# Kernel tuning notes

Measured on AMD Instinct MI355X. Metric: run time of the kernel, lower is better.

## Reference

```python
import jax, jax.numpy as jnp
import numpy as np

D_MODEL = 512
NHEAD = 4
HEAD_DIM = D_MODEL // NHEAD


def setup_inputs() -> dict:
    key = jax.random.key(0)
    ks = jax.random.split(key, 12)
    B, S = 2, 4096
    s = 1.0 / np.sqrt(D_MODEL)
    inp = {
        "query": jax.random.normal(ks[0], (B, S, D_MODEL), jnp.float32),
        "key": jax.random.normal(ks[1], (B, S, D_MODEL), jnp.float32),
        "value": jax.random.normal(ks[2], (B, S, D_MODEL), jnp.float32),
        "Wq": jax.random.uniform(ks[3], (D_MODEL, D_MODEL), jnp.float32, -s, s),
        "bq": jax.random.uniform(ks[4], (D_MODEL,), jnp.float32, -s, s),
        "Wk": jax.random.uniform(ks[5], (D_MODEL, D_MODEL), jnp.float32, -s, s),
        "bk": jax.random.uniform(ks[6], (D_MODEL,), jnp.float32, -s, s),
        "Wv": jax.random.uniform(ks[7], (D_MODEL, D_MODEL), jnp.float32, -s, s),
        "bv": jax.random.uniform(ks[8], (D_MODEL,), jnp.float32, -s, s),
        "Wo": jax.random.uniform(ks[9], (D_MODEL, D_MODEL), jnp.float32, -s, s),
        "bo": jax.random.uniform(ks[10], (D_MODEL,), jnp.float32, -s, s),
    }
    return inp


def reference(query, key, value, Wq, bq, Wk, bk, Wv, bv, Wo, bo):
    B, Sq, _ = query.shape
    Sk = key.shape[1]
    # projections (torch Linear: x @ W.T + b); split heads -> [B, H, S, hd]
    def proj(x, W, b, S):
        return (x @ W.T + b).reshape(B, S, NHEAD, HEAD_DIM).transpose(0, 2, 1, 3)
    Q = proj(query, Wq, bq, Sq)
    K = proj(key, Wk, bk, Sk)
    V = proj(value, Wv, bv, Sk)
    scale = 1.0 / np.sqrt(HEAD_DIM).astype(np.float32)
    scores = jnp.einsum("bhqd,bhkd->bhqk", Q, K) * scale  # [B,H,Sq,Sk]
    weights = jax.nn.softmax(scores, axis=-1)
    out = jnp.einsum("bhqk,bhkd->bhqd", weights, V)  # [B,H,Sq,hd]
    out = out.transpose(0, 2, 1, 3).reshape(B, Sq, D_MODEL)
    return out @ Wo.T + bo
```

## Files before the change

kernel.cpp:

```cpp
#include <hip/hip_runtime.h>


#define D_MODEL 512
#define NHEAD 4
#define HD 128
#define S_ 4096

typedef __attribute__((ext_vector_type(8))) short bf16x8;
typedef __attribute__((ext_vector_type(4))) short bf16x4;
typedef __attribute__((ext_vector_type(4))) float f32x4;
typedef __attribute__((ext_vector_type(2))) unsigned uint2v;
typedef __attribute__((ext_vector_type(4))) unsigned uint4v;

__device__ __forceinline__ short f2bf(float f) {
    unsigned u = __builtin_bit_cast(unsigned, f);
    u += 0x7fffu + ((u >> 16) & 1u);
    return (short)(u >> 16);
}
__device__ __forceinline__ unsigned pk2bf(float a, float b) {
    unsigned ua = __builtin_bit_cast(unsigned, a);
    ua += 0x7fffu + ((ua >> 16) & 1u);
    unsigned ub = __builtin_bit_cast(unsigned, b);
    ub += 0x7fffu + ((ub >> 16) & 1u);
    return (ua >> 16) | (ub & 0xffff0000u);
}

__global__ __launch_bounds__(256) void convert_kernel(
    const float* __restrict__ s0, const float* __restrict__ s1,
    const float* __restrict__ s2, const float* __restrict__ s3,
    const float* __restrict__ s4, const float* __restrict__ s5,
    const float* __restrict__ s6,
    short* __restrict__ d0, short* __restrict__ d1, short* __restrict__ d2,
    short* __restrict__ d3, short* __restrict__ d4, short* __restrict__ d5,
    short* __restrict__ d6)
{
    int seg = blockIdx.y;
    const float* src; short* dst; int n;
    const int NBIG = 2 * S_ * D_MODEL;
    const int NW = D_MODEL * D_MODEL;
    switch (seg) {
        case 0: src = s0; dst = d0; n = NBIG; break;
        case 1: src = s1; dst = d1; n = NBIG; break;
        case 2: src = s2; dst = d2; n = NBIG; break;
        case 3: src = s3; dst = d3; n = NW; break;
        case 4: src = s4; dst = d4; n = NW; break;
        case 5: src = s5; dst = d5; n = NW; break;
        default: src = s6; dst = d6; n = NW; break;
    }
    int idx = (blockIdx.x * 256 + threadIdx.x) * 8;
    if (idx >= n) return;
    float4 a = *(const float4*)(src + idx);
    float4 b = *(const float4*)(src + idx + 4);
    uint4v o;
    o[0] = pk2bf(a.x, a.y); o[1] = pk2bf(a.z, a.w);
    o[2] = pk2bf(b.x, b.y); o[3] = pk2bf(b.z, b.w);
    *(uint4v*)(dst + idx) = o;
}

__global__ __launch_bounds__(256) void qkv_kernel(
    const short* __restrict__ qb, const short* __restrict__ kb,
    const short* __restrict__ vb,
    const short* __restrict__ Wqb, const short* __restrict__ Wkb,
    const short* __restrict__ Wvb,
    const float* __restrict__ bq, const float* __restrict__ bk,
    const float* __restrict__ bv,
    short* __restrict__ Qh, short* __restrict__ Kh, short* __restrict__ VT)
{
    __shared__ short lA[64 * 64];
    __shared__ short lB[128 * 64];
    int z = blockIdx.z;
    const short* A    = (z == 0) ? qb  : (z == 1) ? kb  : vb;
    const short* W    = (z == 0) ? Wqb : (z == 1) ? Wkb : Wvb;
    const float* bias = (z == 0) ? bq  : (z == 1) ? bk  : bv;
    short* out        = (z == 0) ? Qh  : (z == 1) ? Kh  : VT;
    int vmode = (z == 2);

    int t = threadIdx.x;
    int wv = t >> 6, ln = t & 63, q4 = ln >> 4, c = ln & 15;
    int m0 = blockIdx.x * 64, n0 = blockIdx.y * 128;
    f32x4 acc[8] = {};

    for (int k0 = 0; k0 < 512; k0 += 64) {
        for (int i = 0; i < 2; ++i) {
            int id = i * 256 + t;
            int m = id >> 3, kg = id & 7;
            bf16x8 va = *(const bf16x8*)(A + (size_t)(m0 + m) * 512 + k0 + kg * 8);
            *(bf16x8*)&lA[m * 64 + ((kg ^ (m & 7)) << 3)] = va;
        }
        for (int i = 0; i < 4; ++i) {
            int id = i * 256 + t;
            int n = id >> 3, kg = id & 7;
            bf16x8 vb8 = *(const bf16x8*)(W + (size_t)(n0 + n) * 512 + k0 + kg * 8);
            *(bf16x8*)&lB[n * 64 + ((kg ^ (n & 7)) << 3)] = vb8;
        }
        __syncthreads();
        for (int ks = 0; ks < 2; ++ks) {
            int kg = ks * 4 + q4;
            int m = wv * 16 + c;
            bf16x8 af = *(bf16x8*)&lA[m * 64 + ((kg ^ (m & 7)) << 3)];
            bf16x8 bfr[8];
            for (int nt = 0; nt < 8; ++nt) {
                int n = nt * 16 + c;
                bfr[nt] = *(bf16x8*)&lB[n * 64 + ((kg ^ (n & 7)) << 3)];
            }
            for (int nt = 0; nt < 8; ++nt)
                acc[nt] = __builtin_amdgcn_mfma_f32_16x16x32_bf16(af, bfr[nt], acc[nt], 0, 0, 0);
        }
        __syncthreads();
    }

    if (vmode == 0) {
        for (int nt = 0; nt < 8; ++nt) {
            int col = n0 + nt * 16 + c;
            float bv_ = bias[col];
            int h = col >> 7, d = col & 127;
            for (int r = 0; r < 4; ++r) {
                int mrow = m0 + wv * 16 + q4 * 4 + r;
                int b = mrow >> 12, s = mrow & 4095;
                out[((size_t)((b * NHEAD + h) * S_ + s)) * HD + d] = f2bf(acc[nt][r] + bv_);
            }
        }
    } else {
        for (int nt = 0; nt < 8; ++nt) {
            int d = nt * 16 + c;
            float bv_ = bias[n0 + d];
            uint2v pv;
            pv[0] = pk2bf(acc[nt][0] + bv_, acc[nt][1] + bv_);
            pv[1] = pk2bf(acc[nt][2] + bv_, acc[nt][3] + bv_);
            int gr = wv * 4 + q4;
            *(uint2v*)&lB[d * 64 + ((gr ^ (d & 15)) << 2)] = pv;
        }
        __syncthreads();
        int b = m0 >> 12, sbase = m0 & 4095, h = blockIdx.y;
        for (int i = 0; i < 8; ++i) {
            int id = i * 256 + t;
            int d = id >> 4, grl = id & 15;
            bf16x4 v = *(bf16x4*)&lB[d * 64 + ((grl ^ (d & 15)) << 2)];
            *(bf16x4*)&out[((size_t)((b * NHEAD + h) * HD + d)) * S_ + sbase + grl * 4] = v;
        }
    }
}

__global__ __launch_bounds__(256) void outproj_kernel(
    const short* __restrict__ A, const short* __restrict__ W,
    const float* __restrict__ bias, float* __restrict__ out)
{
    __shared__ short lA[64 * 64];
    __shared__ short lB[128 * 64];
    int t = threadIdx.x;
    int wv = t >> 6, ln = t & 63, q4 = ln >> 4, c = ln & 15;
    int m0 = blockIdx.x * 64, n0 = blockIdx.y * 128;
    f32x4 acc[8] = {};

    for (int k0 = 0; k0 < 512; k0 += 64) {
        for (int i = 0; i < 2; ++i) {
            int id = i * 256 + t;
            int m = id >> 3, kg = id & 7;
            bf16x8 va = *(const bf16x8*)(A + (size_t)(m0 + m) * 512 + k0 + kg * 8);
            *(bf16x8*)&lA[m * 64 + ((kg ^ (m & 7)) << 3)] = va;
        }
        for (int i = 0; i < 4; ++i) {
            int id = i * 256 + t;
            int n = id >> 3, kg = id & 7;
            bf16x8 vb8 = *(const bf16x8*)(W + (size_t)(n0 + n) * 512 + k0 + kg * 8);
            *(bf16x8*)&lB[n * 64 + ((kg ^ (n & 7)) << 3)] = vb8;
        }
        __syncthreads();
        for (int ks = 0; ks < 2; ++ks) {
            int kg = ks * 4 + q4;
            int m = wv * 16 + c;
            bf16x8 af = *(bf16x8*)&lA[m * 64 + ((kg ^ (m & 7)) << 3)];
            bf16x8 bfr[8];
            for (int nt = 0; nt < 8; ++nt) {
                int n = nt * 16 + c;
                bfr[nt] = *(bf16x8*)&lB[n * 64 + ((kg ^ (n & 7)) << 3)];
            }
            for (int nt = 0; nt < 8; ++nt)
                acc[nt] = __builtin_amdgcn_mfma_f32_16x16x32_bf16(af, bfr[nt], acc[nt], 0, 0, 0);
        }
        __syncthreads();
    }

    for (int nt = 0; nt < 8; ++nt) {
        int col = n0 + nt * 16 + c;
        float bv_ = bias[col];
        for (int r = 0; r < 4; ++r) {
            int mrow = m0 + wv * 16 + q4 * 4 + r;
            out[(size_t)mrow * 512 + col] = acc[nt][r] + bv_;
        }
    }
}

__global__ __launch_bounds__(256, 2) void flash_kernel(
    const short* __restrict__ Qh, const short* __restrict__ Kh,
    const short* __restrict__ VTg, short* __restrict__ AO,
    float* __restrict__ U, float* __restrict__ ML, int nsplit, int kkspan)
{
    __shared__ short lK[64 * 128];
    __shared__ short lVT[128 * 64];
    __shared__ short lP[128 * 64];
    __shared__ float lL[2][128];
    int t = threadIdx.x;
    int wv = t >> 6, ln = t & 63, q4 = ln >> 4, c = ln & 15;
    int wi = wv >> 1, wj = wv & 1;
    int bh = blockIdx.x;
    int s0 = blockIdx.y * 128;
    int z = blockIdx.z;
    const size_t base = (size_t)bh * S_ * HD;
    const float SC = 0.08838834764831845f * 1.4426950408889634f;

    bf16x8 qf[4][4];
    for (int qt = 0; qt < 4; ++qt) {
        int s = s0 + wi * 64 + qt * 16 + c;
        const short* qp = Qh + base + (size_t)s * HD + q4 * 8;
        for (int ks = 0; ks < 4; ++ks)
            qf[qt][ks] = *(const bf16x8*)(qp + ks * 32);
    }

    f32x4 of[4][4] = {};
    float lrun[4] = {};

    int kkbeg = z * kkspan, kkend = kkbeg + kkspan;

    bf16x8 pkv[4], pvv[4];
    {
        int kk0 = kkbeg;
        for (int i = 0; i < 4; ++i) {
            int id = i * 256 + t;
            int m = id >> 4, kg = id & 15;
            pkv[i] = *(const bf16x8*)(Kh + base + (size_t)(kk0 + m) * HD + kg * 8);
            int mv = id >> 3, kgv = id & 7;
            pvv[i] = *(const bf16x8*)(VTg + base + (size_t)mv * S_ + kk0 + kgv * 8);
        }
    }

    for (int kk0 = kkbeg; kk0 < kkend; kk0 += 64) {
        for (int i = 0; i < 4; ++i) {
            int id = i * 256 + t;
            int m = id >> 4, kg = id & 15;
            *(bf16x8*)&lK[m * 128 + ((kg ^ (m & 7)) << 3)] = pkv[i];
            int mv = id >> 3, kgv = id & 7;
            *(bf16x8*)&lVT[mv * 64 + ((kgv ^ (mv & 7)) << 3)] = pvv[i];
        }
        __syncthreads();

        f32x4 sf[4][2] = {};
        for (int ks = 0; ks < 4; ++ks) {
            int kg = ks * 4 + q4;
            bf16x8 af[2];
            for (int kt = 0; kt < 2; ++kt) {
                int row = wj * 32 + kt * 16 + c;
                af[kt] = *(bf16x8*)&lK[row * 128 + ((kg ^ (row & 7)) << 3)];
            }
            for (int qt = 0; qt < 4; ++qt)
                for (int kt = 0; kt < 2; ++kt)
                    sf[qt][kt] = __builtin_amdgcn_mfma_f32_16x16x32_bf16(
                        af[kt], qf[qt][ks], sf[qt][kt], 0, 0, 0);
        }

        for (int qt = 0; qt < 4; ++qt) {
            float lt = 0.f;
            int row = wi * 64 + qt * 16 + c;
            for (int kt = 0; kt < 2; ++kt) {
                float p0 = exp2f(sf[qt][kt][0] * SC);
                float p1 = exp2f(sf[qt][kt][1] * SC);
                float p2 = exp2f(sf[qt][kt][2] * SC);
                float p3 = exp2f(sf[qt][kt][3] * SC);
                lt += (p0 + p1) + (p2 + p3);
                uint2v pv;
                pv[0] = pk2bf(p0, p1);
                pv[1] = pk2bf(p2, p3);
                int g = wj * 4 + kt * 2 + (q4 >> 1);
                *(uint2v*)&lP[row * 64 + ((g ^ (row & 7)) << 3) + ((q4 & 1) << 2)] = pv;
            }
            lt += __shfl_xor(lt, 16);
            lt += __shfl_xor(lt, 32);
            if (q4 == 0) lL[wj][wi * 64 + qt * 16 + c] = lt;
        }
        __syncthreads();

        for (int qt = 0; qt < 4; ++qt) {
            int q = wi * 64 + qt * 16 + c;
            lrun[qt] += lL[0][q] + lL[1][q];
        }

        if (kk0 + 64 < kkend) {
            int kn = kk0 + 64;
            for (int i = 0; i < 4; ++i) {
                int id = i * 256 + t;
                int m = id >> 4, kg = id & 15;
                pkv[i] = *(const bf16x8*)(Kh + base + (size_t)(kn + m) * HD + kg * 8);
                int mv = id >> 3, kgv = id & 7;
                pvv[i] = *(const bf16x8*)(VTg + base + (size_t)mv * S_ + kn + kgv * 8);
            }
        }

        for (int ksv = 0; ksv < 2; ++ksv) {
            int kg = ksv * 4 + q4;
            bf16x8 av[4], bp[4];
            for (int dt = 0; dt < 4; ++dt) {
                int row = wj * 64 + dt * 16 + c;
                av[dt] = *(bf16x8*)&lVT[row * 64 + ((kg ^ (row & 7)) << 3)];
            }
            for (int qt = 0; qt < 4; ++qt) {
                int row = wi * 64 + qt * 16 + c;
                bp[qt] = *(bf16x8*)&lP[row * 64 + ((kg ^ (row & 7)) << 3)];
            }
            for (int qt = 0; qt < 4; ++qt)
                for (int dt = 0; dt < 4; ++dt)
                    of[dt][qt] = __builtin_amdgcn_mfma_f32_16x16x32_bf16(
                        av[dt], bp[qt], of[dt][qt], 0, 0, 0);
        }
        __syncthreads();
    }

    if (nsplit > 1) {
        for (int qt = 0; qt < 4; ++qt) {
            int s = s0 + wi * 64 + qt * 16 + c;
            size_t rowu = (size_t)(z * 8 + bh) * S_ + s;
            float* up = U + rowu * HD;
            for (int dt = 0; dt < 4; ++dt)
                *(f32x4*)&up[wj * 64 + dt * 16 + q4 * 4] = of[dt][qt];
            if (q4 == 0 && wj == 0) ML[rowu] = lrun[qt];
        }
    } else {
        int b = bh >> 2, h = bh & 3;
        for (int qt = 0; qt < 4; ++qt) {
            float inv = 1.0f / lrun[qt];
            int s = s0 + wi * 64 + qt * 16 + c;
            short* dst = AO + ((size_t)(b * S_ + s)) * D_MODEL + h * HD;
            for (int dt = 0; dt < 4; ++dt) {
                uint2v ov;
                ov[0] = pk2bf(of[dt][qt][0] * inv, of[dt][qt][1] * inv);
                ov[1] = pk2bf(of[dt][qt][2] * inv, of[dt][qt][3] * inv);
                *(uint2v*)(dst + wj * 64 + dt * 16 + q4 * 4) = ov;
            }
        }
    }
}

__global__ __launch_bounds__(256) void combine_kernel(
    const float* __restrict__ U, const float* __restrict__ ML,
    short* __restrict__ AO)
{
    int row = blockIdx.x * 8 + (threadIdx.x >> 5);
    int d4 = (threadIdx.x & 31) * 4;
    const int R = 8 * S_;
    float l = ML[row] + ML[(size_t)R + row];
    float inv = 1.0f / l;
    f32x4 u0 = *(const f32x4*)&U[(size_t)row * HD + d4];
    f32x4 u1 = *(const f32x4*)&U[((size_t)R + row) * HD + d4];
    uint2v o;
    o[0] = pk2bf((u0[0] + u1[0]) * inv, (u0[1] + u1[1]) * inv);
    o[1] = pk2bf((u0[2] + u1[2]) * inv, (u0[3] + u1[3]) * inv);
    int bh = row >> 12, s = row & 4095;
    int b = bh >> 2, h = bh & 3;
    *(uint2v*)&AO[((size_t)(b * S_ + s)) * D_MODEL + h * HD + d4] = o;
}

extern "C" void kernel_launch(void* const* d_in, const int* in_sizes, int n_in,
                              void* d_out, int out_size, void* d_ws, size_t ws_size,
                              hipStream_t stream) {
    const float* q  = (const float*)d_in[0];
    const float* k  = (const float*)d_in[1];
    const float* v  = (const float*)d_in[2];
    const float* Wq = (const float*)d_in[3];
    const float* bq = (const float*)d_in[4];
    const float* Wk = (const float*)d_in[5];
    const float* bk = (const float*)d_in[6];
    const float* Wv = (const float*)d_in[7];
    const float* bv = (const float*)d_in[8];
    const float* Wo = (const float*)d_in[9];
    const float* bo = (const float*)d_in[10];

    const size_t HS = (size_t)2 * NHEAD * S_ * HD;
    const size_t NBIG = HS;
    const size_t NW = (size_t)D_MODEL * D_MODEL;

    char* wsb = (char*)d_ws;
    short* Qh = (short*)wsb;
    short* Kh = Qh + HS;
    short* VT = Kh + HS;
    short* AO = VT + HS;
    char* r2 = wsb + 4 * HS * 2;
    short* qb  = (short*)r2;
    short* kb  = qb + NBIG;
    short* vb  = kb + NBIG;
    short* Wqb = vb + NBIG;
    short* Wkb = Wqb + NW;
    short* Wvb = Wkb + NW;
    float* U   = (float*)r2;
    size_t r2sz = 2 * HS * 4;
    float* ML  = (float*)(r2 + r2sz);
    short* Wob = (short*)((char*)ML + (size_t)2 * 8 * S_ * 4);
    const size_t NEED = 4 * HS * 2 + r2sz + (size_t)2 * 8 * S_ * 4 + NW * 2;

    int nsplit = (ws_size >= NEED) ? 2 : 1;
    int kkspan = S_ / nsplit;

    dim3 blk(256);
    convert_kernel<<<dim3(2048, 7), blk, 0, stream>>>(
        q, k, v, Wq, Wk, Wv, Wo, qb, kb, vb, Wqb, Wkb, Wvb, Wob);
    qkv_kernel<<<dim3(128, 4, 3), blk, 0, stream>>>(
        qb, kb, vb, Wqb, Wkb, Wvb, bq, bk, bv, Qh, Kh, VT);
    flash_kernel<<<dim3(8, 32, nsplit), blk, 0, stream>>>(
        Qh, Kh, VT, AO, U, ML, nsplit, kkspan);
    if (nsplit == 2)
        combine_kernel<<<dim3(S_), blk, 0, stream>>>(U, ML, AO);
    outproj_kernel<<<dim3(128, 4), blk, 0, stream>>>(AO, Wob, bo, (float*)d_out);
}
```

Before: 267.8 us.

## Load GEMM and attention tiles directly into LDS via global_load_lds

Replaces the register-staged global-to-LDS copies in the projection GEMMs and the attention K/V tile loads with direct global_load_lds 16-byte transfers. The XOR swizzle moves from the LDS store address to the global source address. This also drops the register prefetch of the next K/V tile in attention, which removes the overlap of loads with compute. The Q/K projection epilogue now stages results through LDS so it can write coalesced 16-byte rows. The aim is lower VGPR pressure and fewer instructions, at the risk of exposing load latency in the attention loop.

```diff
diff --git a/kernel.cpp b/kernel.cpp
--- a/kernel.cpp
+++ b/kernel.cpp
@@ -23,6 +23,11 @@
     unsigned ub = __builtin_bit_cast(unsigned, b);
     ub += 0x7fffu + ((ub >> 16) & 1u);
     return (ua >> 16) | (ub & 0xffff0000u);
+}
+__device__ __forceinline__ void gl2lds16(const short* g, short* l) {
+    __builtin_amdgcn_global_load_lds(
+        (const __attribute__((address_space(1))) void*)g,
+        (__attribute__((address_space(3))) void*)l, 16, 0, 0);
 }
 
 __global__ __launch_bounds__(256) void convert_kernel(
@@ -66,8 +71,9 @@
     const float* __restrict__ bv,
     short* __restrict__ Qh, short* __restrict__ Kh, short* __restrict__ VT)
 {
-    __shared__ short lA[64 * 64];
-    __shared__ short lB[128 * 64];
+    __shared__ short smem[12288];
+    short* lA = smem;
+    short* lB = smem + 4096;
     int z = blockIdx.z;
     const short* A    = (z == 0) ? qb  : (z == 1) ? kb  : vb;
     const short* W    = (z == 0) ? Wqb : (z == 1) ? Wkb : Wvb;
@@ -83,15 +89,15 @@
     for (int k0 = 0; k0 < 512; k0 += 64) {
         for (int i = 0; i < 2; ++i) {
             int id = i * 256 + t;
-            int m = id >> 3, kg = id & 7;
-            bf16x8 va = *(const bf16x8*)(A + (size_t)(m0 + m) * 512 + k0 + kg * 8);
-            *(bf16x8*)&lA[m * 64 + ((kg ^ (m & 7)) << 3)] = va;
+            int m = id >> 3, kgp = id & 7;
+            gl2lds16(A + (size_t)(m0 + m) * 512 + k0 + ((kgp ^ (m & 7)) << 3),
+                     &lA[id * 8]);
         }
         for (int i = 0; i < 4; ++i) {
             int id = i * 256 + t;
-            int n = id >> 3, kg = id & 7;
-            bf16x8 vb8 = *(const bf16x8*)(W + (size_t)(n0 + n) * 512 + k0 + kg * 8);
-            *(bf16x8*)&lB[n * 64 + ((kg ^ (n & 7)) << 3)] = vb8;
+            int n = id >> 3, kgp = id & 7;
+            gl2lds16(W + (size_t)(n0 + n) * 512 + k0 + ((kgp ^ (n & 7)) << 3),
+                     &lB[id * 8]);
         }
         __syncthreads();
         for (int ks = 0; ks < 2; ++ks) {
@@ -110,15 +116,22 @@
     }
 
     if (vmode == 0) {
+        const int TS = 136;
+        short* lT = smem;
         for (int nt = 0; nt < 8; ++nt) {
-            int col = n0 + nt * 16 + c;
-            float bv_ = bias[col];
-            int h = col >> 7, d = col & 127;
+            float bv_ = bias[n0 + nt * 16 + c];
             for (int r = 0; r < 4; ++r) {
-                int mrow = m0 + wv * 16 + q4 * 4 + r;
-                int b = mrow >> 12, s = mrow & 4095;
-                out[((size_t)((b * NHEAD + h) * S_ + s)) * HD + d] = f2bf(acc[nt][r] + bv_);
-            }
+                int srow = wv * 16 + q4 * 4 + r;
+                lT[srow * TS + nt * 16 + c] = f2bf(acc[nt][r] + bv_);
+            }
+        }
+        __syncthreads();
+        int bb = m0 >> 12, sbase = m0 & 4095, h = blockIdx.y;
+        for (int i = 0; i < 4; ++i) {
+            int id = i * 256 + t;
+            int row = id >> 4, g = id & 15;
+            bf16x8 vv = *(bf16x8*)&lT[row * TS + g * 8];
+            *(bf16x8*)&out[((size_t)((bb * NHEAD + h) * S_ + sbase + row)) * HD + g * 8] = vv;
         }
     } else {
         for (int nt = 0; nt < 8; ++nt) {
@@ -131,12 +144,12 @@
             *(uint2v*)&lB[d * 64 + ((gr ^ (d & 15)) << 2)] = pv;
         }
         __syncthreads();
-        int b = m0 >> 12, sbase = m0 & 4095, h = blockIdx.y;
+        int bb = m0 >> 12, sbase = m0 & 4095, h = blockIdx.y;
         for (int i = 0; i < 8; ++i) {
             int id = i * 256 + t;
             int d = id >> 4, grl = id & 15;
             bf16x4 v = *(bf16x4*)&lB[d * 64 + ((grl ^ (d & 15)) << 2)];
-            *(bf16x4*)&out[((size_t)((b * NHEAD + h) * HD + d)) * S_ + sbase + grl * 4] = v;
+            *(bf16x4*)&out[((size_t)((bb * NHEAD + h) * HD + d)) * S_ + sbase + grl * 4] = v;
         }
     }
 }
@@ -155,15 +168,15 @@
     for (int k0 = 0; k0 < 512; k0 += 64) {
         for (int i = 0; i < 2; ++i) {
             int id = i * 256 + t;
-            int m = id >> 3, kg = id & 7;
-            bf16x8 va = *(const bf16x8*)(A + (size_t)(m0 + m) * 512 + k0 + kg * 8);
-            *(bf16x8*)&lA[m * 64 + ((kg ^ (m & 7)) << 3)] = va;
+            int m = id >> 3, kgp = id & 7;
+            gl2lds16(A + (size_t)(m0 + m) * 512 + k0 + ((kgp ^ (m & 7)) << 3),
+                     &lA[id * 8]);
         }
         for (int i = 0; i < 4; ++i) {
             int id = i * 256 + t;
-            int n = id >> 3, kg = id & 7;
-            bf16x8 vb8 = *(const bf16x8*)(W + (size_t)(n0 + n) * 512 + k0 + kg * 8);
-            *(bf16x8*)&lB[n * 64 + ((kg ^ (n & 7)) << 3)] = vb8;
+            int n = id >> 3, kgp = id & 7;
+            gl2lds16(W + (size_t)(n0 + n) * 512 + k0 + ((kgp ^ (n & 7)) << 3),
+                     &lB[id * 8]);
         }
         __syncthreads();
         for (int ks = 0; ks < 2; ++ks) {
@@ -221,26 +234,15 @@
     float lrun[4] = {};
 
     int kkbeg = z * kkspan, kkend = kkbeg + kkspan;
-
-    bf16x8 pkv[4], pvv[4];
-    {
-        int kk0 = kkbeg;
-        for (int i = 0; i < 4; ++i) {
-            int id = i * 256 + t;
-            int m = id >> 4, kg = id & 15;
-            pkv[i] = *(const bf16x8*)(Kh + base + (size_t)(kk0 + m) * HD + kg * 8);
-            int mv = id >> 3, kgv = id & 7;
-            pvv[i] = *(const bf16x8*)(VTg + base + (size_t)mv * S_ + kk0 + kgv * 8);
-        }
-    }
-
     for (int kk0 = kkbeg; kk0 < kkend; kk0 += 64) {
         for (int i = 0; i < 4; ++i) {
             int id = i * 256 + t;
-            int m = id >> 4, kg = id & 15;
-            *(bf16x8*)&lK[m * 128 + ((kg ^ (m & 7)) << 3)] = pkv[i];
-            int mv = id >> 3, kgv = id & 7;
-            *(bf16x8*)&lVT[mv * 64 + ((kgv ^ (mv & 7)) << 3)] = pvv[i];
+            int m = id >> 4, kgp = id & 15;
+            gl2lds16(Kh + base + (size_t)(kk0 + m) * HD + ((kgp ^ (m & 7)) << 3),
+                     &lK[id * 8]);
+            int mv = id >> 3, kgvp = id & 7;
+            gl2lds16(VTg + base + (size_t)mv * S_ + kk0 + ((kgvp ^ (mv & 7)) << 3),
+                     &lVT[id * 8]);
         }
         __syncthreads();
 
@@ -282,17 +284,6 @@
         for (int qt = 0; qt < 4; ++qt) {
             int q = wi * 64 + qt * 16 + c;
             lrun[qt] += lL[0][q] + lL[1][q];
-        }
-
-        if (kk0 + 64 < kkend) {
-            int kn = kk0 + 64;
-            for (int i = 0; i < 4; ++i) {
-                int id = i * 256 + t;
-                int m = id >> 4, kg = id & 15;
-                pkv[i] = *(const bf16x8*)(Kh + base + (size_t)(kn + m) * HD + kg * 8);
-                int mv = id >> 3, kgv = id & 7;
-                pvv[i] = *(const bf16x8*)(VTg + base + (size_t)mv * S_ + kn + kgv * 8);
-            }
         }
 
         for (int ksv = 0; ksv < 2; ++ksv) {
```

Result: faster. 260.3 us (-2.8%).
